# Performance work log

Hardware: AMD Instinct MI355X
Metric: run time of the kernel (lower is better)

The kernel has to match this reference:

```python
import jax, jax.numpy as jnp
import numpy as np

N, E, G = 200000, 800000, 8000
NODE_IN, EDGE_IN, H = 256, 64, 256


def _mlp2(h, w1, b1, w2, b2):
    return jax.nn.relu(h @ w1 + b1) @ w2 + b2


def setup_inputs() -> dict:
    key = jax.random.key(0)
    ks = jax.random.split(key, 30)
    s = 0.05
    p = lambda k, shp: (jax.random.normal(k, shp, jnp.float32) * s)
    inp = {
        "x": jax.random.normal(ks[0], (N, NODE_IN), jnp.float32),
        "edge_attr": jax.random.normal(ks[1], (E, EDGE_IN), jnp.float32),
        "edge_index": jax.random.randint(ks[2], (2, E), 0, N, dtype=jnp.int32),
        "batch": jnp.sort(jax.random.randint(ks[3], (N,), 0, G, dtype=jnp.int32)),
        # edge MLP
        "em_w1": p(ks[4], (EDGE_IN, H)), "em_b1": jnp.zeros((H,), jnp.float32),
        "em_w2": p(ks[5], (H, H)), "em_b2": jnp.zeros((H,), jnp.float32),
        # GINEConv 1 MLP
        "c1_w1": p(ks[6], (NODE_IN, H)), "c1_b1": jnp.zeros((H,), jnp.float32),
        "c1_w2": p(ks[7], (H, H)), "c1_b2": jnp.zeros((H,), jnp.float32),
        # GINEConv 2 MLP
        "c2_w1": p(ks[8], (H, H)), "c2_b1": jnp.zeros((H,), jnp.float32),
        "c2_w2": p(ks[9], (H, H)), "c2_b2": jnp.zeros((H,), jnp.float32),
        # heads
        "l1_w": p(ks[10], (H, 128)), "l1_b": jnp.zeros((128,), jnp.float32),
        "l2_w": p(ks[11], (128, 64)), "l2_b": jnp.zeros((64,), jnp.float32),
        "hS_w": p(ks[12], (64, 1)), "hS_b": jnp.zeros((1,), jnp.float32),
        "hP_w": p(ks[13], (64, 1)), "hP_b": jnp.zeros((1,), jnp.float32),
        "hN_w": p(ks[14], (64, 1)), "hN_b": jnp.zeros((1,), jnp.float32),
    }
    return inp


def _gine(x, ea, src, dst, w1, b1, w2, b2):
    # GINEConv (eps=0): out = MLP(x_i + sum_j relu(x_j + e_ji))
    msg = jax.nn.relu(x[src] + ea)                      # [E, H]
    agg = jax.ops.segment_sum(msg, dst, num_segments=x.shape[0])
    return _mlp2(x + agg, w1, b1, w2, b2)


def reference(x, edge_attr, edge_index, batch,
              em_w1, em_b1, em_w2, em_b2,
              c1_w1, c1_b1, c1_w2, c1_b2,
              c2_w1, c2_b1, c2_w2, c2_b2,
              l1_w, l1_b, l2_w, l2_b,
              hS_w, hS_b, hP_w, hP_b, hN_w, hN_b):
    src, dst = edge_index[0], edge_index[1]  # source_to_target flow
    ea = _mlp2(edge_attr, em_w1, em_b1, em_w2, em_b2)   # [E, 256]
    h = jax.nn.relu(_gine(x, ea, src, dst, c1_w1, c1_b1, c1_w2, c1_b2))
    h = jax.nn.relu(_gine(h, ea, src, dst, c2_w1, c2_b1, c2_w2, c2_b2))
    # global mean pool over graphs (dropout is identity in eval mode)
    sums = jax.ops.segment_sum(h, batch, num_segments=G)              # [G, 256]
    cnts = jax.ops.segment_sum(jnp.ones((h.shape[0],), h.dtype), batch, num_segments=G)
    pooled = sums / jnp.maximum(cnts, 1.0)[:, None]
    g = jax.nn.relu(pooled @ l1_w + l1_b)
    g = jax.nn.relu(g @ l2_w + l2_b)
    return ((g @ hS_w + hS_b).squeeze(-1),
            (g @ hP_w + hP_b).squeeze(-1),
            (g @ hN_w + hN_b).squeeze(-1))
```

## Files before the change

kernel.cpp:

```cpp
#include <hip/hip_runtime.h>
#include <hip/hip_bf16.h>

typedef __attribute__((ext_vector_type(8))) short short8;
typedef __attribute__((ext_vector_type(4))) float f32x4;
typedef __attribute__((ext_vector_type(2))) unsigned int u32x2;
typedef __attribute__((ext_vector_type(4))) unsigned int u32x4;

#define N_NODES  200000
#define N_EDGES  800000
#define N_GRAPHS 8000

__device__ __forceinline__ unsigned short f2bf(float f) {
  unsigned int u = __float_as_uint(f);
  unsigned int r = (u + 0x7fffu + ((u >> 16) & 1u)) >> 16;
  return (unsigned short)r;
}
__device__ __forceinline__ float bf2f(unsigned short s) {
  return __uint_as_float(((unsigned int)s) << 16);
}
__device__ __forceinline__ unsigned cvtpk(float a, float b) {
  union { __hip_bfloat162 h; unsigned u; } cv;
  cv.h = __float22bfloat162_rn(make_float2(a, b));
  return cv.u;
}

__device__ __forceinline__ void xpose4(unsigned W0, unsigned W1, int bsub,
                                       unsigned selT, unsigned& T0, unsigned& T1) {
  unsigned t0 = (unsigned)__shfl_xor((int)W0, 2);
  unsigned t1 = (unsigned)__shfl_xor((int)W1, 2);
  unsigned A0 = (bsub & 2) ? t1 : W0;
  unsigned A1 = (bsub & 2) ? W1 : t0;
  unsigned t2 = (unsigned)__shfl_xor((int)A0, 1);
  unsigned t3 = (unsigned)__shfl_xor((int)A1, 1);
  T0 = __builtin_amdgcn_perm(A0, t2, selT);
  T1 = __builtin_amdgcn_perm(A1, t3, selT);
}

__global__ void wtrans(const float* __restrict__ w, unsigned short* __restrict__ wt,
                       int K, int Nc) {
  int id = blockIdx.x * 256 + threadIdx.x;
  if (id >= K * Nc) return;
  int k = id / Nc, n = id % Nc;
  wt[n * K + k] = f2bf(w[id]);
}

template <int K1, int IN_MODE>
__global__ __launch_bounds__(256) void fused_mlp2(
    const float* __restrict__ Xf, const unsigned short* __restrict__ Xb,
    const unsigned short* __restrict__ aggb,
    const unsigned short* __restrict__ w1t, const float* __restrict__ b1,
    const unsigned short* __restrict__ w2t, const float* __restrict__ b2,
    unsigned short* __restrict__ out, int relu_out) {
  constexpr int SLAB  = (K1 < 128) ? K1 : 128;
  constexpr int NSLAB = K1 / SLAB;
  constexpr int NKK   = SLAB / 32;
  __shared__ unsigned short a_lds[64 * SLAB];
  __shared__ unsigned short h_lds[64 * 256];
  char* abase = (char*)a_lds;
  char* hbase = (char*)h_lds;

  const int tid  = threadIdx.x;
  const int row0 = blockIdx.x * 64;
  const int lane = tid & 63;
  const int wid  = tid >> 6;
  const int lr   = lane & 15;
  const int kq   = lane >> 4;
  const int col0 = wid * 64;
  const int bsub = lr & 3;
  const int asub = lr >> 2;
  const unsigned selT = (bsub & 1) ? 0x07060302u : 0x01000504u;

  const int srow = tid >> 2;
  const int skk  = (tid & 3) * 8;

  f32x4 acc[4][4];
#pragma unroll
  for (int m = 0; m < 4; ++m)
#pragma unroll
    for (int n = 0; n < 4; ++n) acc[m][n] = (f32x4){0.f, 0.f, 0.f, 0.f};

  float bias1[4];
#pragma unroll
  for (int n = 0; n < 4; ++n) bias1[n] = b1[col0 + n * 16 + lr];

#pragma unroll
  for (int s = 0; s < NSLAB; ++s) {
#pragma unroll
    for (int c2 = 0; c2 < NKK; ++c2) {
      const int kloc = skk + 32 * c2;
      const int gk = s * SLAB + kloc;
      float v[8];
      if (IN_MODE == 0 || IN_MODE == 1) {
        const float* xp = Xf + (size_t)(row0 + srow) * K1 + gk;
        float4 A = *(const float4*)xp;
        float4 B = *(const float4*)(xp + 4);
        v[0]=A.x; v[1]=A.y; v[2]=A.z; v[3]=A.w; v[4]=B.x; v[5]=B.y; v[6]=B.z; v[7]=B.w;
      } else {
        const unsigned short* hp = Xb + (size_t)(row0 + srow) * 256 + gk;
        short8 hv = *(const short8*)hp;
#pragma unroll
        for (int i = 0; i < 8; ++i) v[i] = bf2f((unsigned short)hv[i]);
      }
      if (IN_MODE >= 1) {
        const unsigned short* ap = aggb + (size_t)(row0 + srow) * 256 + gk;
        short8 av = *(const short8*)ap;
#pragma unroll
        for (int i = 0; i < 8; ++i) v[i] += bf2f((unsigned short)av[i]);
      }
      u32x4 pk;
#pragma unroll
      for (int i = 0; i < 4; ++i) pk[i] = cvtpk(v[2 * i], v[2 * i + 1]);
      int ab = srow * (2 * SLAB) + kloc * 2;
      ab ^= (srow & 7) << 4;
      *(u32x4*)(abase + ab) = pk;
    }
    __syncthreads();

#pragma unroll
    for (int kk = 0; kk < NKK; ++kk) {
      short8 af[4], bq[4];
#pragma unroll
      for (int m = 0; m < 4; ++m) {
        int r = m * 16 + lr;
        int off = r * (2 * SLAB) + kk * 64 + kq * 16;
        off ^= (r & 7) << 4;
        af[m] = *(short8*)(abase + off);
      }
#pragma unroll
      for (int n = 0; n < 4; ++n) {
        int c = col0 + n * 16 + lr;
        bq[n] = *(const short8*)(w1t + (size_t)c * K1 + s * SLAB + kk * 32 + kq * 8);
      }
#pragma unroll
      for (int m = 0; m < 4; ++m)
#pragma unroll
        for (int n = 0; n < 4; ++n)
          acc[m][n] = __builtin_amdgcn_mfma_f32_16x16x32_bf16(af[m], bq[n], acc[m][n], 0, 0, 0);
    }
    if (s < NSLAB - 1) __syncthreads();
  }

#pragma unroll
  for (int n = 0; n < 4; ++n) {
    float bn = bias1[n];
#pragma unroll
    for (int m = 0; m < 4; ++m) {
      float v0 = fmaxf(acc[m][n][0] + bn, 0.f);
      float v1 = fmaxf(acc[m][n][1] + bn, 0.f);
      float v2 = fmaxf(acc[m][n][2] + bn, 0.f);
      float v3 = fmaxf(acc[m][n][3] + bn, 0.f);
      unsigned W0 = cvtpk(v0, v1), W1 = cvtpk(v2, v3), T0, T1;
      xpose4(W0, W1, bsub, selT, T0, T1);
      int r = m * 16 + kq * 4 + bsub;
      int cb = col0 + n * 16 + asub * 4;
      int off = r * 512 + cb * 2;
      off ^= (r & 7) << 4;
      *(u32x2*)(hbase + off) = (u32x2){T0, T1};
    }
  }
  __syncthreads();

#pragma unroll
  for (int m = 0; m < 4; ++m)
#pragma unroll
    for (int n = 0; n < 4; ++n) acc[m][n] = (f32x4){0.f, 0.f, 0.f, 0.f};

  float bias2[4];
#pragma unroll
  for (int n = 0; n < 4; ++n) bias2[n] = b2[col0 + n * 16 + lr];

#pragma unroll
  for (int ks = 0; ks < 8; ++ks) {
    short8 af[4], bq[4];
#pragma unroll
    for (int m = 0; m < 4; ++m) {
      int r = m * 16 + lr;
      int off = r * 512 + ks * 64 + kq * 16;
      off ^= (r & 7) << 4;
      af[m] = *(short8*)(hbase + off);
    }
#pragma unroll
    for (int n = 0; n < 4; ++n) {
      int c = col0 + n * 16 + lr;
      bq[n] = *(const short8*)(w2t + (size_t)c * 256 + ks * 32 + kq * 8);
    }
#pragma unroll
    for (int m = 0; m < 4; ++m)
#pragma unroll
      for (int n = 0; n < 4; ++n)
        acc[m][n] = __builtin_amdgcn_mfma_f32_16x16x32_bf16(af[m], bq[n], acc[m][n], 0, 0, 0);
  }
  __syncthreads();

#pragma unroll
  for (int n = 0; n < 4; ++n) {
    float bn = bias2[n];
#pragma unroll
    for (int m = 0; m < 4; ++m) {
      float v0 = acc[m][n][0] + bn;
      float v1 = acc[m][n][1] + bn;
      float v2 = acc[m][n][2] + bn;
      float v3 = acc[m][n][3] + bn;
      if (relu_out) {
        v0 = fmaxf(v0, 0.f); v1 = fmaxf(v1, 0.f);
        v2 = fmaxf(v2, 0.f); v3 = fmaxf(v3, 0.f);
      }
      unsigned W0 = cvtpk(v0, v1), W1 = cvtpk(v2, v3), T0, T1;
      xpose4(W0, W1, bsub, selT, T0, T1);
      int r = m * 16 + kq * 4 + bsub;
      int cb = col0 + n * 16 + asub * 4;
      int off = r * 512 + cb * 2;
      off ^= (r & 7) << 4;
      *(u32x2*)(hbase + off) = (u32x2){T0, T1};
    }
  }
  __syncthreads();

#pragma unroll
  for (int it = 0; it < 8; ++it) {
    int r = (tid >> 5) + it * 8;
    int byte = (tid & 31) * 16;
    int off = (r * 512 + byte) ^ ((r & 7) << 4);
    u32x4 d = *(u32x4*)(hbase + off);
    *(u32x4*)((char*)out + (size_t)(row0 + r) * 512 + byte) = d;
  }
}

__global__ void hist_deg(const int* __restrict__ dst, int* __restrict__ rp) {
  int e = blockIdx.x * 256 + threadIdx.x;
  if (e < N_EDGES) atomicAdd(&rp[dst[e]], 1);
}

__global__ __launch_bounds__(256) void scan_block(int* __restrict__ rp,
                                                  int* __restrict__ bsum) {
  __shared__ int ts[256];
  int b = blockIdx.x, t = threadIdx.x;
  int base = b * 2048 + t * 8;
  int v[8]; int s = 0;
#pragma unroll
  for (int i = 0; i < 8; ++i) {
    int idx = base + i;
    v[i] = (idx < N_NODES) ? rp[idx] : 0;
    s += v[i];
  }
  ts[t] = s;
  __syncthreads();
#pragma unroll
  for (int off = 1; off < 256; off <<= 1) {
    int add = (t >= off) ? ts[t - off] : 0;
    __syncthreads();
    ts[t] += add;
    __syncthreads();
  }
  int excl = ts[t] - s;
  if (t == 255) bsum[b] = ts[255];
  int run = excl;
#pragma unroll
  for (int i = 0; i < 8; ++i) {
    int idx = base + i;
    if (idx < N_NODES) rp[idx] = run;
    run += v[i];
  }
}

__global__ __launch_bounds__(256) void scan_bsum(int* __restrict__ bsum, int nb) {
  __shared__ int ts[256];
  int t = threadIdx.x;
  int v = (t < nb) ? bsum[t] : 0;
  ts[t] = v;
  __syncthreads();
#pragma unroll
  for (int off = 1; off < 256; off <<= 1) {
    int add = (t >= off) ? ts[t - off] : 0;
    __syncthreads();
    ts[t] += add;
    __syncthreads();
  }
  if (t < nb) bsum[t] = ts[t] - v;
}

__global__ void scan_add(int* __restrict__ rp, const int* __restrict__ bsum) {
  int i = blockIdx.x * 256 + threadIdx.x;
  if (i < N_NODES) rp[i] += bsum[i >> 11];
}

__global__ void csr_fill(const int* __restrict__ src, const int* __restrict__ dst,
                         int* __restrict__ rp, int2* __restrict__ csr) {
  int e = blockIdx.x * 256 + threadIdx.x;
  if (e >= N_EDGES) return;
  int d = dst[e];
  int p = atomicAdd(&rp[d], 1);
  csr[p] = make_int2(src[e], e);
}

template <int IN_BF16>
__global__ __launch_bounds__(256) void gather_agg(
    const unsigned short* __restrict__ ea, const float* __restrict__ xf,
    const unsigned short* __restrict__ xb, const int* __restrict__ rp,
    const int2* __restrict__ csr, unsigned short* __restrict__ agg) {
  int v = blockIdx.x * 4 + (threadIdx.x >> 6);
  if (v >= N_NODES) return;
  int lane = threadIdx.x & 63;
  int c = lane * 4;
  int beg = (v == 0) ? 0 : rp[v - 1];
  int end = rp[v];
  float a0 = 0.f, a1 = 0.f, a2 = 0.f, a3 = 0.f;
  int i = beg;
  for (; i + 2 <= end; i += 2) {
    int2 s0 = csr[i];
    int2 s1 = csr[i + 1];
    ushort4 e0 = *(const ushort4*)(ea + (size_t)s0.y * 256 + c);
    ushort4 e1 = *(const ushort4*)(ea + (size_t)s1.y * 256 + c);
    float x00, x01, x02, x03, x10, x11, x12, x13;
    if (IN_BF16) {
      ushort4 h0 = *(const ushort4*)(xb + (size_t)s0.x * 256 + c);
      ushort4 h1 = *(const ushort4*)(xb + (size_t)s1.x * 256 + c);
      x00 = bf2f(h0.x); x01 = bf2f(h0.y); x02 = bf2f(h0.z); x03 = bf2f(h0.w);
      x10 = bf2f(h1.x); x11 = bf2f(h1.y); x12 = bf2f(h1.z); x13 = bf2f(h1.w);
    } else {
      float4 v0 = *(const float4*)(xf + (size_t)s0.x * 256 + c);
      float4 v1 = *(const float4*)(xf + (size_t)s1.x * 256 + c);
      x00 = v0.x; x01 = v0.y; x02 = v0.z; x03 = v0.w;
      x10 = v1.x; x11 = v1.y; x12 = v1.z; x13 = v1.w;
    }
    a0 += fmaxf(x00 + bf2f(e0.x), 0.f) + fmaxf(x10 + bf2f(e1.x), 0.f);
    a1 += fmaxf(x01 + bf2f(e0.y), 0.f) + fmaxf(x11 + bf2f(e1.y), 0.f);
    a2 += fmaxf(x02 + bf2f(e0.z), 0.f) + fmaxf(x12 + bf2f(e1.z), 0.f);
    a3 += fmaxf(x03 + bf2f(e0.w), 0.f) + fmaxf(x13 + bf2f(e1.w), 0.f);
  }
  if (i < end) {
    int2 se = csr[i];
    ushort4 ev = *(const ushort4*)(ea + (size_t)se.y * 256 + c);
    float x0, x1, x2, x3;
    if (IN_BF16) {
      ushort4 hv = *(const ushort4*)(xb + (size_t)se.x * 256 + c);
      x0 = bf2f(hv.x); x1 = bf2f(hv.y); x2 = bf2f(hv.z); x3 = bf2f(hv.w);
    } else {
      float4 xv = *(const float4*)(xf + (size_t)se.x * 256 + c);
      x0 = xv.x; x1 = xv.y; x2 = xv.z; x3 = xv.w;
    }
    a0 += fmaxf(x0 + bf2f(ev.x), 0.f);
    a1 += fmaxf(x1 + bf2f(ev.y), 0.f);
    a2 += fmaxf(x2 + bf2f(ev.z), 0.f);
    a3 += fmaxf(x3 + bf2f(ev.w), 0.f);
  }
  u32x2 pk = {cvtpk(a0, a1), cvtpk(a2, a3)};
  *(u32x2*)(agg + (size_t)v * 256 + c) = pk;
}

__global__ __launch_bounds__(256) void pool_mean(const unsigned short* __restrict__ h2,
                                                 const int* __restrict__ batch,
                                                 float* __restrict__ pooled) {
  int g = blockIdx.x;
  int tid = threadIdx.x;
  int lo = 0, hi = N_NODES;
  while (lo < hi) { int mid = (lo + hi) >> 1; if (batch[mid] < g) lo = mid + 1; else hi = mid; }
  int start = lo;
  hi = N_NODES;
  while (lo < hi) { int mid = (lo + hi) >> 1; if (batch[mid] < g + 1) lo = mid + 1; else hi = mid; }
  int end = lo;
  float s = 0.f;
  for (int r = start; r < end; ++r) s += bf2f(h2[(size_t)r * 256 + tid]);
  float cnt = (float)(end - start);
  pooled[(size_t)g * 256 + tid] = s / fmaxf(cnt, 1.0f);
}

__global__ __launch_bounds__(128) void head_mlp(
    const float* __restrict__ pooled, const float* __restrict__ l1w,
    const float* __restrict__ l1b, const float* __restrict__ l2w,
    const float* __restrict__ l2b, const float* __restrict__ hSw,
    const float* __restrict__ hSb, const float* __restrict__ hPw,
    const float* __restrict__ hPb, const float* __restrict__ hNw,
    const float* __restrict__ hNb, float* __restrict__ out) {
  int g = blockIdx.x, tid = threadIdx.x;
  __shared__ float p[256];
  __shared__ float g1[128];
  __shared__ float g2[64];
  p[tid] = pooled[(size_t)g * 256 + tid];
  p[tid + 128] = pooled[(size_t)g * 256 + tid + 128];
  __syncthreads();
  float a = l1b[tid];
#pragma unroll 8
  for (int k = 0; k < 256; ++k) a += p[k] * l1w[k * 128 + tid];
  g1[tid] = fmaxf(a, 0.f);
  __syncthreads();
  if (tid < 64) {
    float b = l2b[tid];
#pragma unroll 8
    for (int k = 0; k < 128; ++k) b += g1[k] * l2w[k * 64 + tid];
    g2[tid] = fmaxf(b, 0.f);
  }
  __syncthreads();
  if (tid < 64) {
    float v = g2[tid];
    float s = v * hSw[tid], pq = v * hPw[tid], nq = v * hNw[tid];
#pragma unroll
    for (int off = 32; off > 0; off >>= 1) {
      s  += __shfl_down(s, off);
      pq += __shfl_down(pq, off);
      nq += __shfl_down(nq, off);
    }
    if (tid == 0) {
      out[g]                = s  + hSb[0];
      out[N_GRAPHS + g]     = pq + hPb[0];
      out[2 * N_GRAPHS + g] = nq + hNb[0];
    }
  }
}

extern "C" void kernel_launch(void* const* d_in, const int* in_sizes, int n_in,
                              void* d_out, int out_size, void* d_ws, size_t ws_size,
                              hipStream_t stream) {
  const float* x         = (const float*)d_in[0];
  const float* edge_attr = (const float*)d_in[1];
  const int*   ei        = (const int*)d_in[2];
  const int*   batch     = (const int*)d_in[3];
  const float* em_w1 = (const float*)d_in[4];  const float* em_b1 = (const float*)d_in[5];
  const float* em_w2 = (const float*)d_in[6];  const float* em_b2 = (const float*)d_in[7];
  const float* c1_w1 = (const float*)d_in[8];  const float* c1_b1 = (const float*)d_in[9];
  const float* c1_w2 = (const float*)d_in[10]; const float* c1_b2 = (const float*)d_in[11];
  const float* c2_w1 = (const float*)d_in[12]; const float* c2_b1 = (const float*)d_in[13];
  const float* c2_w2 = (const float*)d_in[14]; const float* c2_b2 = (const float*)d_in[15];
  const float* l1_w = (const float*)d_in[16];  const float* l1_b = (const float*)d_in[17];
  const float* l2_w = (const float*)d_in[18];  const float* l2_b = (const float*)d_in[19];
  const float* hS_w = (const float*)d_in[20];  const float* hS_b = (const float*)d_in[21];
  const float* hP_w = (const float*)d_in[22];  const float* hP_b = (const float*)d_in[23];
  const float* hN_w = (const float*)d_in[24];  const float* hN_b = (const float*)d_in[25];

  char* ws = (char*)d_ws;
  unsigned short* ea     = (unsigned short*)ws;
  unsigned short* agg    = (unsigned short*)(ws + 409600000);
  unsigned short* h1     = (unsigned short*)(ws + 614400000);
  unsigned short* h2     = ea;
  float*          pooled = (float*)(ws + 716800000);
  int2*           csr    = (int2*)(ws + 716800000);
  int*            rp     = (int*)(ws + 723200000);
  int*            bsum   = (int*)(ws + 724000000);
  unsigned short* wt     = (unsigned short*)(ws + 724992000);
  unsigned short* em_w1t = wt;
  unsigned short* em_w2t = em_w1t + 16384;
  unsigned short* c1_w1t = em_w2t + 65536;
  unsigned short* c1_w2t = c1_w1t + 65536;
  unsigned short* c2_w1t = c1_w2t + 65536;
  unsigned short* c2_w2t = c2_w1t + 65536;

  const int* srcI = ei;
  const int* dstI = ei + N_EDGES;

  wtrans<<<(16384 + 255) / 256, 256, 0, stream>>>(em_w1, em_w1t, 64, 256);
  wtrans<<<(65536 + 255) / 256, 256, 0, stream>>>(em_w2, em_w2t, 256, 256);
  wtrans<<<(65536 + 255) / 256, 256, 0, stream>>>(c1_w1, c1_w1t, 256, 256);
  wtrans<<<(65536 + 255) / 256, 256, 0, stream>>>(c1_w2, c1_w2t, 256, 256);
  wtrans<<<(65536 + 255) / 256, 256, 0, stream>>>(c2_w1, c2_w1t, 256, 256);
  wtrans<<<(65536 + 255) / 256, 256, 0, stream>>>(c2_w2, c2_w2t, 256, 256);

  hipMemsetAsync(rp, 0, (size_t)N_NODES * 4, stream);
  hist_deg<<<(N_EDGES + 255) / 256, 256, 0, stream>>>(dstI, rp);
  scan_block<<<(N_NODES + 2047) / 2048, 256, 0, stream>>>(rp, bsum);
  scan_bsum<<<1, 256, 0, stream>>>(bsum, (N_NODES + 2047) / 2048);
  scan_add<<<(N_NODES + 255) / 256, 256, 0, stream>>>(rp, bsum);
  csr_fill<<<N_EDGES / 256, 256, 0, stream>>>(srcI, dstI, rp, csr);

  fused_mlp2<64, 0><<<N_EDGES / 64, 256, 0, stream>>>(
      edge_attr, nullptr, nullptr, em_w1t, em_b1, em_w2t, em_b2, ea, 0);

  gather_agg<0><<<(N_NODES + 3) / 4, 256, 0, stream>>>(ea, x, nullptr, rp, csr, agg);
  fused_mlp2<256, 1><<<N_NODES / 64, 256, 0, stream>>>(
      x, nullptr, agg, c1_w1t, c1_b1, c1_w2t, c1_b2, h1, 1);

  gather_agg<1><<<(N_NODES + 3) / 4, 256, 0, stream>>>(ea, nullptr, h1, rp, csr, agg);
  fused_mlp2<256, 2><<<N_NODES / 64, 256, 0, stream>>>(
      nullptr, h1, agg, c2_w1t, c2_b1, c2_w2t, c2_b2, h2, 1);

  pool_mean<<<N_GRAPHS, 256, 0, stream>>>(h2, batch, pooled);
  head_mlp<<<N_GRAPHS, 128, 0, stream>>>(pooled, l1_w, l1_b, l2_w, l2_b,
                                         hS_w, hS_b, hP_w, hP_b, hN_w, hN_b,
                                         (float*)d_out);
}
```

Measured before the change: 1.185 ms.

## Convert x to bf16 once, double-buffer A slabs in h_lds, parallelize pooling

Adds a pre-pass that converts x to bf16 so the first gather and first conv MLP read half the bytes; both now use the bf16 path. The fused MLP drops its separate A-operand LDS buffer and double-buffers slabs inside the h_lds region. This lowers LDS use and allows a launch-bounds occupancy hint of 5, and the next slab is staged before the MFMAs on the current one. Pool_mean now has each wave read vectorized rows and reduces the partial sums through shared memory. The tradeoffs are an extra conversion kernel and x rounded to bf16 earlier than before.

```diff
diff --git a/kernel.cpp b/kernel.cpp
--- a/kernel.cpp
+++ b/kernel.cpp
@@ -44,8 +44,51 @@
   wt[n * K + k] = f2bf(w[id]);
 }
 
+__global__ __launch_bounds__(256) void x2bf(const float* __restrict__ x,
+                                            unsigned short* __restrict__ xb) {
+  int id = blockIdx.x * 256 + threadIdx.x;
+  if (id >= N_NODES * 256 / 8) return;
+  float4 a = ((const float4*)x)[id * 2];
+  float4 b = ((const float4*)x)[id * 2 + 1];
+  u32x4 pk = {cvtpk(a.x, a.y), cvtpk(a.z, a.w), cvtpk(b.x, b.y), cvtpk(b.z, b.w)};
+  ((u32x4*)xb)[id] = pk;
+}
+
+template <int K1, int IN_MODE, int SLAB, int NKK>
+__device__ __forceinline__ void stage_slab(
+    int s, char* ab, int row0, int srow, int skk,
+    const float* __restrict__ Xf, const unsigned short* __restrict__ Xb,
+    const unsigned short* __restrict__ aggb) {
+#pragma unroll
+  for (int c2 = 0; c2 < NKK; ++c2) {
+    const int kloc = skk + 32 * c2;
+    const int gk = s * SLAB + kloc;
+    float v[8];
+    if (IN_MODE == 0) {
+      const float* xp = Xf + (size_t)(row0 + srow) * K1 + gk;
+      float4 A = *(const float4*)xp;
+      float4 B = *(const float4*)(xp + 4);
+      v[0]=A.x; v[1]=A.y; v[2]=A.z; v[3]=A.w; v[4]=B.x; v[5]=B.y; v[6]=B.z; v[7]=B.w;
+    } else {
+      const unsigned short* hp = Xb + (size_t)(row0 + srow) * 256 + gk;
+      short8 hv = *(const short8*)hp;
+      const unsigned short* ap = aggb + (size_t)(row0 + srow) * 256 + gk;
+      short8 av = *(const short8*)ap;
+#pragma unroll
+      for (int i = 0; i < 8; ++i)
+        v[i] = bf2f((unsigned short)hv[i]) + bf2f((unsigned short)av[i]);
+    }
+    u32x4 pk;
+#pragma unroll
+    for (int i = 0; i < 4; ++i) pk[i] = cvtpk(v[2 * i], v[2 * i + 1]);
+    int off = srow * (2 * SLAB) + kloc * 2;
+    off ^= (srow & 7) << 4;
+    *(u32x4*)(ab + off) = pk;
+  }
+}
+
 template <int K1, int IN_MODE>
-__global__ __launch_bounds__(256) void fused_mlp2(
+__global__ __launch_bounds__(256, 5) void fused_mlp2(
     const float* __restrict__ Xf, const unsigned short* __restrict__ Xb,
     const unsigned short* __restrict__ aggb,
     const unsigned short* __restrict__ w1t, const float* __restrict__ b1,
@@ -54,9 +97,7 @@
   constexpr int SLAB  = (K1 < 128) ? K1 : 128;
   constexpr int NSLAB = K1 / SLAB;
   constexpr int NKK   = SLAB / 32;
-  __shared__ unsigned short a_lds[64 * SLAB];
   __shared__ unsigned short h_lds[64 * 256];
-  char* abase = (char*)a_lds;
   char* hbase = (char*)h_lds;
 
   const int tid  = threadIdx.x;
@@ -83,39 +124,15 @@
 #pragma unroll
   for (int n = 0; n < 4; ++n) bias1[n] = b1[col0 + n * 16 + lr];
 
+  stage_slab<K1, IN_MODE, SLAB, NKK>(0, hbase, row0, srow, skk, Xf, Xb, aggb);
+  __syncthreads();
+
 #pragma unroll
   for (int s = 0; s < NSLAB; ++s) {
-#pragma unroll
-    for (int c2 = 0; c2 < NKK; ++c2) {
-      const int kloc = skk + 32 * c2;
-      const int gk = s * SLAB + kloc;
-      float v[8];
-      if (IN_MODE == 0 || IN_MODE == 1) {
-        const float* xp = Xf + (size_t)(row0 + srow) * K1 + gk;
-        float4 A = *(const float4*)xp;
-        float4 B = *(const float4*)(xp + 4);
-        v[0]=A.x; v[1]=A.y; v[2]=A.z; v[3]=A.w; v[4]=B.x; v[5]=B.y; v[6]=B.z; v[7]=B.w;
-      } else {
-        const unsigned short* hp = Xb + (size_t)(row0 + srow) * 256 + gk;
-        short8 hv = *(const short8*)hp;
-#pragma unroll
-        for (int i = 0; i < 8; ++i) v[i] = bf2f((unsigned short)hv[i]);
-      }
-      if (IN_MODE >= 1) {
-        const unsigned short* ap = aggb + (size_t)(row0 + srow) * 256 + gk;
-        short8 av = *(const short8*)ap;
-#pragma unroll
-        for (int i = 0; i < 8; ++i) v[i] += bf2f((unsigned short)av[i]);
-      }
-      u32x4 pk;
-#pragma unroll
-      for (int i = 0; i < 4; ++i) pk[i] = cvtpk(v[2 * i], v[2 * i + 1]);
-      int ab = srow * (2 * SLAB) + kloc * 2;
-      ab ^= (srow & 7) << 4;
-      *(u32x4*)(abase + ab) = pk;
-    }
-    __syncthreads();
-
+    if (s + 1 < NSLAB)
+      stage_slab<K1, IN_MODE, SLAB, NKK>(s + 1, hbase + 16384, row0, srow, skk,
+                                         Xf, Xb, aggb);
+    char* ab = hbase + (s & 1) * 16384;
 #pragma unroll
     for (int kk = 0; kk < NKK; ++kk) {
       short8 af[4], bq[4];
@@ -124,7 +141,7 @@
         int r = m * 16 + lr;
         int off = r * (2 * SLAB) + kk * 64 + kq * 16;
         off ^= (r & 7) << 4;
-        af[m] = *(short8*)(abase + off);
+        af[m] = *(short8*)(ab + off);
       }
 #pragma unroll
       for (int n = 0; n < 4; ++n) {
@@ -137,7 +154,7 @@
         for (int n = 0; n < 4; ++n)
           acc[m][n] = __builtin_amdgcn_mfma_f32_16x16x32_bf16(af[m], bq[n], acc[m][n], 0, 0, 0);
     }
-    if (s < NSLAB - 1) __syncthreads();
+    __syncthreads();
   }
 
 #pragma unroll
@@ -293,11 +310,10 @@
   csr[p] = make_int2(src[e], e);
 }
 
-template <int IN_BF16>
 __global__ __launch_bounds__(256) void gather_agg(
-    const unsigned short* __restrict__ ea, const float* __restrict__ xf,
-    const unsigned short* __restrict__ xb, const int* __restrict__ rp,
-    const int2* __restrict__ csr, unsigned short* __restrict__ agg) {
+    const unsigned short* __restrict__ ea, const unsigned short* __restrict__ xb,
+    const int* __restrict__ rp, const int2* __restrict__ csr,
+    unsigned short* __restrict__ agg) {
   int v = blockIdx.x * 4 + (threadIdx.x >> 6);
   if (v >= N_NODES) return;
   int lane = threadIdx.x & 63;
@@ -311,38 +327,21 @@
     int2 s1 = csr[i + 1];
     ushort4 e0 = *(const ushort4*)(ea + (size_t)s0.y * 256 + c);
     ushort4 e1 = *(const ushort4*)(ea + (size_t)s1.y * 256 + c);
-    float x00, x01, x02, x03, x10, x11, x12, x13;
-    if (IN_BF16) {
-      ushort4 h0 = *(const ushort4*)(xb + (size_t)s0.x * 256 + c);
-      ushort4 h1 = *(const ushort4*)(xb + (size_t)s1.x * 256 + c);
-      x00 = bf2f(h0.x); x01 = bf2f(h0.y); x02 = bf2f(h0.z); x03 = bf2f(h0.w);
-      x10 = bf2f(h1.x); x11 = bf2f(h1.y); x12 = bf2f(h1.z); x13 = bf2f(h1.w);
-    } else {
-      float4 v0 = *(const float4*)(xf + (size_t)s0.x * 256 + c);
-      float4 v1 = *(const float4*)(xf + (size_t)s1.x * 256 + c);
-      x00 = v0.x; x01 = v0.y; x02 = v0.z; x03 = v0.w;
-      x10 = v1.x; x11 = v1.y; x12 = v1.z; x13 = v1.w;
-    }
-    a0 += fmaxf(x00 + bf2f(e0.x), 0.f) + fmaxf(x10 + bf2f(e1.x), 0.f);
-    a1 += fmaxf(x01 + bf2f(e0.y), 0.f) + fmaxf(x11 + bf2f(e1.y), 0.f);
-    a2 += fmaxf(x02 + bf2f(e0.z), 0.f) + fmaxf(x12 + bf2f(e1.z), 0.f);
-    a3 += fmaxf(x03 + bf2f(e0.w), 0.f) + fmaxf(x13 + bf2f(e1.w), 0.f);
+    ushort4 h0 = *(const ushort4*)(xb + (size_t)s0.x * 256 + c);
+    ushort4 h1 = *(const ushort4*)(xb + (size_t)s1.x * 256 + c);
+    a0 += fmaxf(bf2f(h0.x) + bf2f(e0.x), 0.f) + fmaxf(bf2f(h1.x) + bf2f(e1.x), 0.f);
+    a1 += fmaxf(bf2f(h0.y) + bf2f(e0.y), 0.f) + fmaxf(bf2f(h1.y) + bf2f(e1.y), 0.f);
+    a2 += fmaxf(bf2f(h0.z) + bf2f(e0.z), 0.f) + fmaxf(bf2f(h1.z) + bf2f(e1.z), 0.f);
+    a3 += fmaxf(bf2f(h0.w) + bf2f(e0.w), 0.f) + fmaxf(bf2f(h1.w) + bf2f(e1.w), 0.f);
   }
   if (i < end) {
     int2 se = csr[i];
     ushort4 ev = *(const ushort4*)(ea + (size_t)se.y * 256 + c);
-    float x0, x1, x2, x3;
-    if (IN_BF16) {
-      ushort4 hv = *(const ushort4*)(xb + (size_t)se.x * 256 + c);
-      x0 = bf2f(hv.x); x1 = bf2f(hv.y); x2 = bf2f(hv.z); x3 = bf2f(hv.w);
-    } else {
-      float4 xv = *(const float4*)(xf + (size_t)se.x * 256 + c);
-      x0 = xv.x; x1 = xv.y; x2 = xv.z; x3 = xv.w;
-    }
-    a0 += fmaxf(x0 + bf2f(ev.x), 0.f);
-    a1 += fmaxf(x1 + bf2f(ev.y), 0.f);
-    a2 += fmaxf(x2 + bf2f(ev.z), 0.f);
-    a3 += fmaxf(x3 + bf2f(ev.w), 0.f);
+    ushort4 hv = *(const ushort4*)(xb + (size_t)se.x * 256 + c);
+    a0 += fmaxf(bf2f(hv.x) + bf2f(ev.x), 0.f);
+    a1 += fmaxf(bf2f(hv.y) + bf2f(ev.y), 0.f);
+    a2 += fmaxf(bf2f(hv.z) + bf2f(ev.z), 0.f);
+    a3 += fmaxf(bf2f(hv.w) + bf2f(ev.w), 0.f);
   }
   u32x2 pk = {cvtpk(a0, a1), cvtpk(a2, a3)};
   *(u32x2*)(agg + (size_t)v * 256 + c) = pk;
@@ -353,16 +352,31 @@
                                                  float* __restrict__ pooled) {
   int g = blockIdx.x;
   int tid = threadIdx.x;
+  int lane = tid & 63;
+  int sub = tid >> 6;
   int lo = 0, hi = N_NODES;
   while (lo < hi) { int mid = (lo + hi) >> 1; if (batch[mid] < g) lo = mid + 1; else hi = mid; }
   int start = lo;
   hi = N_NODES;
   while (lo < hi) { int mid = (lo + hi) >> 1; if (batch[mid] < g + 1) lo = mid + 1; else hi = mid; }
   int end = lo;
-  float s = 0.f;
-  for (int r = start; r < end; ++r) s += bf2f(h2[(size_t)r * 256 + tid]);
-  float cnt = (float)(end - start);
-  pooled[(size_t)g * 256 + tid] = s / fmaxf(cnt, 1.0f);
+  float s0 = 0.f, s1 = 0.f, s2 = 0.f, s3 = 0.f;
+  for (int r = start + sub; r < end; r += 4) {
+    ushort4 hv = *(const ushort4*)(h2 + (size_t)r * 256 + lane * 4);
+    s0 += bf2f(hv.x); s1 += bf2f(hv.y); s2 += bf2f(hv.z); s3 += bf2f(hv.w);
+  }
+  __shared__ float4 red[4][64];
+  red[sub][lane] = make_float4(s0, s1, s2, s3);
+  __syncthreads();
+  if (sub == 0) {
+    float4 a = red[0][lane], b = red[1][lane], cc = red[2][lane], d = red[3][lane];
+    float inv = 1.0f / fmaxf((float)(end - start), 1.0f);
+    float4 t = make_float4((a.x + b.x + cc.x + d.x) * inv,
+                           (a.y + b.y + cc.y + d.y) * inv,
+                           (a.z + b.z + cc.z + d.z) * inv,
+                           (a.w + b.w + cc.w + d.w) * inv);
+    *(float4*)(pooled + (size_t)g * 256 + lane * 4) = t;
+  }
 }
 
 __global__ __launch_bounds__(128) void head_mlp(
@@ -430,6 +444,7 @@
   char* ws = (char*)d_ws;
   unsigned short* ea     = (unsigned short*)ws;
   unsigned short* agg    = (unsigned short*)(ws + 409600000);
+  unsigned short* xb     = (unsigned short*)(ws + 512000000);
   unsigned short* h1     = (unsigned short*)(ws + 614400000);
   unsigned short* h2     = ea;
   float*          pooled = (float*)(ws + 716800000);
@@ -454,6 +469,8 @@
   wtrans<<<(65536 + 255) / 256, 256, 0, stream>>>(c2_w1, c2_w1t, 256, 256);
   wtrans<<<(65536 + 255) / 256, 256, 0, stream>>>(c2_w2, c2_w2t, 256, 256);
 
+  x2bf<<<(N_NODES * 256 / 8 + 255) / 256, 256, 0, stream>>>(x, xb);
+
   hipMemsetAsync(rp, 0, (size_t)N_NODES * 4, stream);
   hist_deg<<<(N_EDGES + 255) / 256, 256, 0, stream>>>(dstI, rp);
   scan_block<<<(N_NODES + 2047) / 2048, 256, 0, stream>>>(rp, bsum);
@@ -464,11 +481,11 @@
   fused_mlp2<64, 0><<<N_EDGES / 64, 256, 0, stream>>>(
       edge_attr, nullptr, nullptr, em_w1t, em_b1, em_w2t, em_b2, ea, 0);
 
-  gather_agg<0><<<(N_NODES + 3) / 4, 256, 0, stream>>>(ea, x, nullptr, rp, csr, agg);
-  fused_mlp2<256, 1><<<N_NODES / 64, 256, 0, stream>>>(
-      x, nullptr, agg, c1_w1t, c1_b1, c1_w2t, c1_b2, h1, 1);
-
-  gather_agg<1><<<(N_NODES + 3) / 4, 256, 0, stream>>>(ea, nullptr, h1, rp, csr, agg);
+  gather_agg<<<(N_NODES + 3) / 4, 256, 0, stream>>>(ea, xb, rp, csr, agg);
+  fused_mlp2<256, 2><<<N_NODES / 64, 256, 0, stream>>>(
+      nullptr, xb, agg, c1_w1t, c1_b1, c1_w2t, c1_b2, h1, 1);
+
+  gather_agg<<<(N_NODES + 3) / 4, 256, 0, stream>>>(ea, h1, rp, csr, agg);
   fused_mlp2<256, 2><<<N_NODES / 64, 256, 0, stream>>>(
       nullptr, h1, agg, c2_w1t, c2_b1, c2_w2t, c2_b2, h2, 1);
 
```

Result: slower. 2.009 ms (+69.6%).
